# Kernel optimization log

Hardware: AMD Instinct MI355X
Metric: run time of the kernel (lower is better)

## Reference

```python
import jax, jax.numpy as jnp
import numpy as np

N, E, F_IN, H, F_OUT = 50000, 400000, 128, 256, 1
EPS = 1e-5


def setup_inputs() -> dict:
    key = jax.random.key(0)
    ks = jax.random.split(key, 10)
    s = lambda fan_in: 1.0 / np.sqrt(fan_in)
    return {
        "x": jax.random.normal(ks[0], (N, F_IN), dtype=jnp.float32),
        "edge_index": jax.random.randint(ks[1], (2, E), 0, N, dtype=jnp.int64),
        # gcn1: GCNConv(F_IN -> H) + BatchNorm1d(H) params
        "W1": jax.random.uniform(ks[2], (F_IN, H), jnp.float32, -s(F_IN), s(F_IN)),
        "b1": jnp.zeros((H,), jnp.float32),
        "gamma": jnp.ones((H,), jnp.float32),
        "beta": jnp.zeros((H,), jnp.float32),
        # gcn2: GCNConv(H -> H)
        "W2": jax.random.uniform(ks[3], (H, H), jnp.float32, -s(H), s(H)),
        "b2": jnp.zeros((H,), jnp.float32),
        # ClassifierMLP2(2H -> F_OUT): Linear(2H, H) -> ReLU -> Linear(H, F_OUT)
        "Wm1": jax.random.uniform(ks[4], (2 * H, H), jnp.float32, -s(2 * H), s(2 * H)),
        "bm1": jnp.zeros((H,), jnp.float32),
        "Wm2": jax.random.uniform(ks[5], (H, F_OUT), jnp.float32, -s(H), s(H)),
        "bm2": jnp.zeros((F_OUT,), jnp.float32),
    }


def _gcn_conv(x, W, b, src_full, dst_full, norm):
    # x' = D^{-1/2} (A + I) D^{-1/2} X W + b   (self loops already appended)
    xw = x @ W                                  # [N, H]
    msg = xw[src_full] * norm[:, None]          # [E+N, H] gather + scale
    agg = jax.ops.segment_sum(msg, dst_full, num_segments=N)  # scatter-add
    return agg + b


def reference(x, edge_index, W1, b1, gamma, beta, W2, b2, Wm1, bm1, Wm2, bm2):
    src, dst = edge_index[0], edge_index[1]
    loop = jnp.arange(N, dtype=edge_index.dtype)
    src_full = jnp.concatenate([src, loop])     # add_self_loops
    dst_full = jnp.concatenate([dst, loop])
    deg = jax.ops.segment_sum(jnp.ones_like(dst_full, dtype=x.dtype), dst_full,
                              num_segments=N)   # degree of A + I (>= 1)
    dinv = jax.lax.rsqrt(deg)
    norm = dinv[src_full] * dinv[dst_full]      # [E+N] symmetric norm

    # gcn1: conv -> batchnorm (batch stats) -> relu
    h = _gcn_conv(x, W1, b1, src_full, dst_full, norm)
    mu = jnp.mean(h, axis=0)
    var = jnp.mean(jnp.square(h - mu), axis=0)  # biased var, as in BN forward
    h = (h - mu) * jax.lax.rsqrt(var + EPS) * gamma + beta
    h = jax.nn.relu(h)

    # gcn2: conv -> relu
    h = jax.nn.relu(_gcn_conv(h, W2, b2, src_full, dst_full, norm))

    # mix_node_features 'cat': per-edge concat of endpoint features
    edges_x = jnp.concatenate([h[src], h[dst]], axis=-1)  # [E, 2H]

    # ClassifierMLP2 + sigmoid
    out = jax.nn.relu(edges_x @ Wm1 + bm1) @ Wm2 + bm2
    return jax.nn.sigmoid(out)                  # [E, 1]
```

## Files before the change

### kernel.cpp

```cpp
#include <hip/hip_runtime.h>
#include <math.h>

#define NN 50000
#define EE 400000
#define FIN 128
#define HH 256
#define BN_EPS 1e-5f
#define NSB 196

typedef __attribute__((ext_vector_type(8))) short short8v;
typedef __attribute__((ext_vector_type(4))) short short4v;
typedef __attribute__((ext_vector_type(2))) short short2v;
typedef __attribute__((ext_vector_type(4))) float f32x4;

__device__ inline short f2bf(float x) {
    union { float f; unsigned u; } c; c.f = x;
    unsigned r = c.u + 0x7FFF + ((c.u >> 16) & 1);
    return (short)(r >> 16);
}
__device__ inline float bf2f(short b) {
    union { unsigned u; float f; } c; c.u = ((unsigned)(unsigned short)b) << 16;
    return c.f;
}


__global__ void k_count(const int* __restrict__ dst, int* __restrict__ cnt) {
    int e = blockIdx.x * 256 + threadIdx.x;
    if (e < EE) atomicAdd(&cnt[dst[e]], 1);
}

__global__ __launch_bounds__(256) void k_scan1(const int* __restrict__ cnt,
                                               int* __restrict__ bsum) {
    __shared__ int ws4[4];
    int i = blockIdx.x * 256 + threadIdx.x;
    int s = (i < NN) ? cnt[i] : 0;
#pragma unroll
    for (int o = 32; o; o >>= 1) s += __shfl_down(s, o);
    if ((threadIdx.x & 63) == 0) ws4[threadIdx.x >> 6] = s;
    __syncthreads();
    if (threadIdx.x == 0) bsum[blockIdx.x] = ws4[0] + ws4[1] + ws4[2] + ws4[3];
}

__global__ __launch_bounds__(256) void k_scan2(const int* __restrict__ bsum,
                                               int* __restrict__ boff,
                                               int* __restrict__ row_start) {
    __shared__ int sh[256];
    int t = threadIdx.x;
    int v = (t < NSB) ? bsum[t] : 0;
    sh[t] = v;
    __syncthreads();
    for (int o = 1; o < 256; o <<= 1) {
        int u = (t >= o) ? sh[t - o] : 0;
        __syncthreads();
        sh[t] += u;
        __syncthreads();
    }
    if (t < NSB) boff[t] = sh[t] - v;
    if (t == 0) row_start[NN] = EE;
}

__global__ __launch_bounds__(256) void k_scan3(const int* __restrict__ cnt,
                                               const int* __restrict__ boff,
                                               int* __restrict__ row_start,
                                               int* __restrict__ cursor,
                                               float* __restrict__ dinv) {
    __shared__ int sh[256];
    int t = threadIdx.x;
    int i = blockIdx.x * 256 + t;
    int v = (i < NN) ? cnt[i] : 0;
    sh[t] = v;
    __syncthreads();
    for (int o = 1; o < 256; o <<= 1) {
        int u = (t >= o) ? sh[t - o] : 0;
        __syncthreads();
        sh[t] += u;
        __syncthreads();
    }
    if (i < NN) {
        int rs = boff[blockIdx.x] + sh[t] - v;
        row_start[i] = rs;
        cursor[i] = rs;
        dinv[i] = rsqrtf((float)(v + 1));
    }
}

__global__ void k_fill(const int* __restrict__ src, const int* __restrict__ dst,
                       int* __restrict__ cursor, int* __restrict__ csr_src) {
    int e = blockIdx.x * 256 + threadIdx.x;
    if (e < EE) {
        int pos = atomicAdd(&cursor[dst[e]], 1);
        csr_src[pos] = src[e];
    }
}


__global__ void k_wsplit(const float* __restrict__ src, short* __restrict__ hi,
                         short* __restrict__ lo, int K, int NC) {
    int i = blockIdx.x * 256 + threadIdx.x;
    if (i >= K * NC) return;
    int k = i / NC, n = i - k * NC;
    float v = src[i];
    short h = f2bf(v);
    short lw = f2bf(v - bf2f(h));
    size_t d = ((size_t)(k >> 3) * NC + n) * 8 + (k & 7);
    hi[d] = h;
    lo[d] = lw;
}

__global__ void k_wsplit_cat(const float* __restrict__ Wm1, short* __restrict__ hi,
                             short* __restrict__ lo) {
    int i = blockIdx.x * 256 + threadIdx.x;
    if (i >= 256 * 512) return;
    int k = i >> 9, c = i & 511;
    float v = (c < 256) ? Wm1[k * 256 + c] : Wm1[(256 + k) * 256 + (c - 256)];
    short h = f2bf(v);
    short lw = f2bf(v - bf2f(h));
    size_t d = ((size_t)(k >> 3) * 512 + c) * 8 + (k & 7);
    hi[d] = h;
    lo[d] = lw;
}


__global__ __launch_bounds__(256) void k_aggX(const float* __restrict__ x,
                                              const int* __restrict__ csr_src,
                                              const int* __restrict__ row_start,
                                              const float* __restrict__ dinv,
                                              short* __restrict__ Ghi,
                                              short* __restrict__ Glo) {
    int wave = threadIdx.x >> 6, lane = threadIdx.x & 63;
    int n = blockIdx.x * 4 + wave;
    if (n >= NN) return;
    const float2* base = reinterpret_cast<const float2*>(x);
    float g = dinv[n];
    float2 v = base[(size_t)n * 64 + lane];
    v.x *= g; v.y *= g;
    int s0 = row_start[n], s1 = row_start[n + 1];
    for (int j = s0; j < s1; ++j) {
        int sj = csr_src[j];
        float gj = dinv[sj];
        float2 u = base[(size_t)sj * 64 + lane];
        v.x += gj * u.x; v.y += gj * u.y;
    }
    v.x *= g; v.y *= g;
    short2v h, lw;
    short h0 = f2bf(v.x), h1 = f2bf(v.y);
    h[0] = h0; h[1] = h1;
    lw[0] = f2bf(v.x - bf2f(h0)); lw[1] = f2bf(v.y - bf2f(h1));
    *(short2v*)(Ghi + (size_t)n * FIN + lane * 2) = h;
    *(short2v*)(Glo + (size_t)n * FIN + lane * 2) = lw;
}

__global__ __launch_bounds__(256) void k_aggH(const float* __restrict__ T,
                                              const int* __restrict__ csr_src,
                                              const int* __restrict__ row_start,
                                              const float* __restrict__ dinv,
                                              short* __restrict__ Ghi,
                                              short* __restrict__ Glo) {
    int wave = threadIdx.x >> 6, lane = threadIdx.x & 63;
    int n = blockIdx.x * 4 + wave;
    if (n >= NN) return;
    const float4* base = reinterpret_cast<const float4*>(T);
    float4 v = base[(size_t)n * 64 + lane];
    int s0 = row_start[n], s1 = row_start[n + 1];
    for (int j = s0; j < s1; ++j) {
        float4 u = base[(size_t)csr_src[j] * 64 + lane];
        v.x += u.x; v.y += u.y; v.z += u.z; v.w += u.w;
    }
    float g = dinv[n];
    float o[4] = {v.x * g, v.y * g, v.z * g, v.w * g};
    short4v h, lw;
#pragma unroll
    for (int j = 0; j < 4; ++j) {
        short hh = f2bf(o[j]);
        h[j] = hh;
        lw[j] = f2bf(o[j] - bf2f(hh));
    }
    *(short4v*)(Ghi + (size_t)n * HH + lane * 4) = h;
    *(short4v*)(Glo + (size_t)n * HH + lane * 4) = lw;
}


template<int K, int NC, int EPI>
__global__ __launch_bounds__(256, 2) void gemm_stripe(
    const short* __restrict__ Ahi, const short* __restrict__ Alo,
    const short* __restrict__ Bthi, const short* __restrict__ Btlo,
    const float* __restrict__ bias,
    float* __restrict__ OutF, short* __restrict__ OutH, short* __restrict__ OutL,
    short* __restrict__ OutA, short* __restrict__ OutB2, int M)
{
    constexpr int NKT = K / 32;
    constexpr int NSLAB = K / 8;
    constexpr int NPASS = NC / 64;
    __shared__ short lds[2 * NSLAB * 512];
    const int tid = threadIdx.x;
    const int w = tid >> 6, l = tid & 63;
    const int wr = w >> 1, wc = w & 1;
    const int m0 = blockIdx.x * 64;
    const int lhi = l >> 4, llo = l & 15;

    for (int s = w; s < 2 * NSLAB; s += 4) {
        int kg = (s < NSLAB) ? s : (s - NSLAB);
        const short* srcp = (s < NSLAB) ? Ahi : Alo;
        int row = m0 + l;
        if (row > M - 1) row = M - 1;
        short8v v = *(const short8v*)(srcp + (size_t)row * K + kg * 8);
        *(short8v*)(&lds[s * 512 + l * 8]) = v;
    }
    __syncthreads();

    for (int pass = 0; pass < NPASS; ++pass) {
        const int n0 = pass * 64 + wc * 32;
        f32x4 acc[2][2] = {};
#pragma unroll
        for (int kt = 0; kt < NKT; ++kt) {
            short8v bh[2], bl[2];
#pragma unroll
            for (int nt = 0; nt < 2; ++nt) {
                size_t idx = ((size_t)(kt * 4 + lhi) * NC + (n0 + nt * 16 + llo)) * 8;
                bh[nt] = *(const short8v*)(Bthi + idx);
                bl[nt] = *(const short8v*)(Btlo + idx);
            }
            short8v ah[2], al[2];
#pragma unroll
            for (int mt = 0; mt < 2; ++mt) {
                int off = (kt * 4 + lhi) * 512 + (wr * 32 + mt * 16 + llo) * 8;
                ah[mt] = *(const short8v*)(&lds[off]);
                al[mt] = *(const short8v*)(&lds[off + NSLAB * 512]);
            }
#pragma unroll
            for (int mt = 0; mt < 2; ++mt)
#pragma unroll
                for (int nt = 0; nt < 2; ++nt) {
                    acc[mt][nt] = __builtin_amdgcn_mfma_f32_16x16x32_bf16(ah[mt], bh[nt], acc[mt][nt], 0, 0, 0);
                    acc[mt][nt] = __builtin_amdgcn_mfma_f32_16x16x32_bf16(ah[mt], bl[nt], acc[mt][nt], 0, 0, 0);
                    acc[mt][nt] = __builtin_amdgcn_mfma_f32_16x16x32_bf16(al[mt], bh[nt], acc[mt][nt], 0, 0, 0);
                }
        }
#pragma unroll
        for (int mt = 0; mt < 2; ++mt)
#pragma unroll
            for (int r = 0; r < 4; ++r) {
                int gm = m0 + wr * 32 + mt * 16 + lhi * 4 + r;
                if (gm >= M) continue;
#pragma unroll
                for (int nt = 0; nt < 2; ++nt) {
                    int col = n0 + nt * 16 + llo;
                    float v = acc[mt][nt][r];
                    if constexpr (EPI == 0) {
                        OutF[(size_t)gm * NC + col] = v + bias[col];
                    } else if constexpr (EPI == 1) {
                        float o = fmaxf(v + bias[col], 0.0f);
                        short h = f2bf(o);
                        OutH[(size_t)gm * NC + col] = h;
                        OutL[(size_t)gm * NC + col] = f2bf(o - bf2f(h));
                    } else {
                        short h = f2bf(v);
                        if (col < NC / 2)
                            OutA[(size_t)gm * (NC / 2) + col] = h;
                        else
                            OutB2[(size_t)gm * (NC / 2) + col - NC / 2] = h;
                    }
                }
            }
    }
}


__global__ __launch_bounds__(256) void k_bn_stats(const float* __restrict__ Hm,
                                                  float* __restrict__ ssum,
                                                  float* __restrict__ ssq) {
    int c = threadIdx.x;
    int r0 = blockIdx.x * 64;
    int r1 = min(r0 + 64, NN);
    float s = 0.f, q = 0.f;
    for (int r = r0; r < r1; ++r) {
        float v = Hm[(size_t)r * HH + c];
        s += v;
        q += v * v;
    }
    atomicAdd(&ssum[c], s);
    atomicAdd(&ssq[c], q);
}

__global__ void k_bn_final(const float* __restrict__ ssum, const float* __restrict__ ssq,
                           const float* __restrict__ gamma, const float* __restrict__ beta,
                           float* __restrict__ scale, float* __restrict__ shift) {
    int c = threadIdx.x;
    float mu = ssum[c] / (float)NN;
    float var = ssq[c] / (float)NN - mu * mu;
    float rstd = rsqrtf(var + BN_EPS);
    float sc = rstd * gamma[c];
    scale[c] = sc;
    shift[c] = beta[c] - mu * sc;
}

__global__ void k_bn_apply_T(const float* __restrict__ P1, const float* __restrict__ scale,
                             const float* __restrict__ shift, const float* __restrict__ dinv,
                             float* __restrict__ T) {
    int i4 = blockIdx.x * 256 + threadIdx.x;
    if (i4 >= NN * HH / 4) return;
    int c4 = i4 & 63;
    float g = dinv[i4 >> 6];
    float4 v = reinterpret_cast<const float4*>(P1)[i4];
    float4 sc = reinterpret_cast<const float4*>(scale)[c4];
    float4 sh = reinterpret_cast<const float4*>(shift)[c4];
    v.x = g * fmaxf(v.x * sc.x + sh.x, 0.f);
    v.y = g * fmaxf(v.y * sc.y + sh.y, 0.f);
    v.z = g * fmaxf(v.z * sc.z + sh.z, 0.f);
    v.w = g * fmaxf(v.w * sc.w + sh.w, 0.f);
    reinterpret_cast<float4*>(T)[i4] = v;
}


__global__ __launch_bounds__(256) void k_edge(const short* __restrict__ Aarr,
                                              const short* __restrict__ Barr,
                                              const int* __restrict__ src,
                                              const int* __restrict__ dst,
                                              const float* __restrict__ bm1,
                                              const float* __restrict__ Wm2,
                                              const float* __restrict__ bm2,
                                              float* __restrict__ out) {
    int wave = threadIdx.x >> 6;
    int lane = threadIdx.x & 63;
    int e = blockIdx.x * 4 + wave;
    if (e >= EE) return;
    int s = src[e], d = dst[e];
    short4v a = *(const short4v*)(Aarr + (size_t)s * 256 + lane * 4);
    short4v b = *(const short4v*)(Barr + (size_t)d * 256 + lane * 4);
    float4 bb = reinterpret_cast<const float4*>(bm1)[lane];
    float4 w = reinterpret_cast<const float4*>(Wm2)[lane];
    float t = fmaxf(bf2f(a[0]) + bf2f(b[0]) + bb.x, 0.f) * w.x
            + fmaxf(bf2f(a[1]) + bf2f(b[1]) + bb.y, 0.f) * w.y
            + fmaxf(bf2f(a[2]) + bf2f(b[2]) + bb.z, 0.f) * w.z
            + fmaxf(bf2f(a[3]) + bf2f(b[3]) + bb.w, 0.f) * w.w;
#pragma unroll
    for (int off = 32; off; off >>= 1) t += __shfl_xor(t, off);
    if (lane == 0) {
        float z = t + bm2[0];
        out[e] = 1.0f / (1.0f + expf(-z));
    }
}


extern "C" void kernel_launch(void* const* d_in, const int* in_sizes, int n_in,
                              void* d_out, int out_size, void* d_ws, size_t ws_size,
                              hipStream_t stream) {
    const float* x     = (const float*)d_in[0];
    const int*   ei    = (const int*)d_in[1];
    const float* W1    = (const float*)d_in[2];
    const float* b1    = (const float*)d_in[3];
    const float* gamma = (const float*)d_in[4];
    const float* beta  = (const float*)d_in[5];
    const float* W2    = (const float*)d_in[6];
    const float* b2    = (const float*)d_in[7];
    const float* Wm1   = (const float*)d_in[8];
    const float* bm1   = (const float*)d_in[9];
    const float* Wm2   = (const float*)d_in[10];
    const float* bm2   = (const float*)d_in[11];
    float* out = (float*)d_out;
    const int* src = ei;
    const int* dst = ei + EE;

    char* ws = (char*)d_ws;
    size_t off = 0;
    auto take = [&](size_t b) -> char* {
        char* p = ws + off;
        off += (b + 255) & ~(size_t)255;
        return p;
    };
    int*   deg_cnt   = (int*)take((size_t)NN * 4);
    float* dinv      = (float*)take((size_t)NN * 4);
    int*   row_start = (int*)take((size_t)(NN + 1) * 4);
    int*   cursor    = (int*)take((size_t)NN * 4);
    int*   csr_src   = (int*)take((size_t)EE * 4);
    int*   bsum      = (int*)take((size_t)NSB * 4);
    int*   boff      = (int*)take((size_t)NSB * 4);
    float* ssum      = (float*)take(1024);
    float* ssq       = (float*)take(1024);
    float* scale     = (float*)take(1024);
    float* shift     = (float*)take(1024);
    short* W1thi     = (short*)take((size_t)128 * 256 * 2);
    short* W1tlo     = (short*)take((size_t)128 * 256 * 2);
    short* W2thi     = (short*)take((size_t)256 * 256 * 2);
    short* W2tlo     = (short*)take((size_t)256 * 256 * 2);
    short* Wcthi     = (short*)take((size_t)256 * 512 * 2);
    short* Wctlo     = (short*)take((size_t)256 * 512 * 2);
    const size_t SLOT = (size_t)NN * HH * 4;
    char* slotA = take(SLOT);
    char* slotB = take(SLOT);
    char* slotC = take(SLOT);

    short* G1hi = (short*)slotB;
    short* G1lo = (short*)(slotB + 12800000);
    float* P1   = (float*)slotC;
    float* T    = (float*)slotA;
    short* G2hi = (short*)slotB;
    short* G2lo = (short*)(slotB + 25600000);
    short* H2hi = (short*)slotC;
    short* H2lo = (short*)(slotC + 25600000);
    short* Aarr = (short*)slotA;
    short* Barr = (short*)(slotA + 25600000);
    (void)ssq; (void)ws_size;

    hipMemsetAsync(deg_cnt, 0, (size_t)NN * 4, stream);
    hipMemsetAsync(ssum, 0, 2048, stream);

    k_count<<<(EE + 255) / 256, 256, 0, stream>>>(dst, deg_cnt);
    k_scan1<<<NSB, 256, 0, stream>>>(deg_cnt, bsum);
    k_scan2<<<1, 256, 0, stream>>>(bsum, boff, row_start);
    k_scan3<<<NSB, 256, 0, stream>>>(deg_cnt, boff, row_start, cursor, dinv);
    k_fill<<<(EE + 255) / 256, 256, 0, stream>>>(src, dst, cursor, csr_src);
    k_wsplit<<<(128 * 256 + 255) / 256, 256, 0, stream>>>(W1, W1thi, W1tlo, 128, 256);
    k_wsplit<<<(256 * 256 + 255) / 256, 256, 0, stream>>>(W2, W2thi, W2tlo, 256, 256);
    k_wsplit_cat<<<(256 * 512 + 255) / 256, 256, 0, stream>>>(Wm1, Wcthi, Wctlo);

    const int MB = (NN + 63) / 64;
    k_aggX<<<(NN + 3) / 4, 256, 0, stream>>>(x, csr_src, row_start, dinv, G1hi, G1lo);
    gemm_stripe<128, 256, 0><<<MB, 256, 0, stream>>>(G1hi, G1lo, W1thi, W1tlo, b1,
                                                     P1, nullptr, nullptr, nullptr, nullptr, NN);
    k_bn_stats<<<(NN + 63) / 64, 256, 0, stream>>>(P1, ssum, ssq);
    k_bn_final<<<1, 256, 0, stream>>>(ssum, ssq, gamma, beta, scale, shift);
    k_bn_apply_T<<<NN * HH / 4 / 256, 256, 0, stream>>>(P1, scale, shift, dinv, T);
    k_aggH<<<(NN + 3) / 4, 256, 0, stream>>>(T, csr_src, row_start, dinv, G2hi, G2lo);
    gemm_stripe<256, 256, 1><<<MB, 256, 0, stream>>>(G2hi, G2lo, W2thi, W2tlo, b2,
                                                     nullptr, H2hi, H2lo, nullptr, nullptr, NN);
    gemm_stripe<256, 512, 2><<<MB, 256, 0, stream>>>(H2hi, H2lo, Wcthi, Wctlo, nullptr,
                                                     nullptr, nullptr, nullptr, Aarr, Barr, NN);
    k_edge<<<(EE + 3) / 4, 256, 0, stream>>>(Aarr, Barr, src, dst, bm1, Wm2, bm2, out);
}
```

Measured before the change: 546.0 us.

## Store CSR edge ids, iterate edges per destination node, shrink GEMM row tile

The CSR now stores original edge ids instead of source ids, so the final edge classifier can walk edges grouped by destination node. The destination-side projection and bias are then loaded once per node instead of once per edge. The GEMM row tile drops from 64 to 32 rows, with each of four waves covering a 32-column stripe, and launch bounds are raised to target higher occupancy. The cost is an extra indirection (srcl[csr_eid[j]]) in both aggregation kernels and scattered per-edge output writes.

Result: slower. 677.6 us (+24.1%).

```diff
diff --git a/kernel.cpp b/kernel.cpp
--- a/kernel.cpp
+++ b/kernel.cpp
@@ -84,12 +84,12 @@
     }
 }
 
-__global__ void k_fill(const int* __restrict__ src, const int* __restrict__ dst,
-                       int* __restrict__ cursor, int* __restrict__ csr_src) {
+__global__ void k_fill(const int* __restrict__ dst,
+                       int* __restrict__ cursor, int* __restrict__ csr_eid) {
     int e = blockIdx.x * 256 + threadIdx.x;
     if (e < EE) {
         int pos = atomicAdd(&cursor[dst[e]], 1);
-        csr_src[pos] = src[e];
+        csr_eid[pos] = e;
     }
 }
 
@@ -122,7 +122,8 @@
 
 
 __global__ __launch_bounds__(256) void k_aggX(const float* __restrict__ x,
-                                              const int* __restrict__ csr_src,
+                                              const int* __restrict__ srcl,
+                                              const int* __restrict__ csr_eid,
                                               const int* __restrict__ row_start,
                                               const float* __restrict__ dinv,
                                               short* __restrict__ Ghi,
@@ -136,7 +137,7 @@
     v.x *= g; v.y *= g;
     int s0 = row_start[n], s1 = row_start[n + 1];
     for (int j = s0; j < s1; ++j) {
-        int sj = csr_src[j];
+        int sj = srcl[csr_eid[j]];
         float gj = dinv[sj];
         float2 u = base[(size_t)sj * 64 + lane];
         v.x += gj * u.x; v.y += gj * u.y;
@@ -151,7 +152,8 @@
 }
 
 __global__ __launch_bounds__(256) void k_aggH(const float* __restrict__ T,
-                                              const int* __restrict__ csr_src,
+                                              const int* __restrict__ srcl,
+                                              const int* __restrict__ csr_eid,
                                               const int* __restrict__ row_start,
                                               const float* __restrict__ dinv,
                                               short* __restrict__ Ghi,
@@ -163,7 +165,8 @@
     float4 v = base[(size_t)n * 64 + lane];
     int s0 = row_start[n], s1 = row_start[n + 1];
     for (int j = s0; j < s1; ++j) {
-        float4 u = base[(size_t)csr_src[j] * 64 + lane];
+        int sj = srcl[csr_eid[j]];
+        float4 u = base[(size_t)sj * 64 + lane];
         v.x += u.x; v.y += u.y; v.z += u.z; v.w += u.w;
     }
     float g = dinv[n];
@@ -181,7 +184,7 @@
 
 
 template<int K, int NC, int EPI>
-__global__ __launch_bounds__(256, 2) void gemm_stripe(
+__global__ __launch_bounds__(256, 4) void gemm_stripe(
     const short* __restrict__ Ahi, const short* __restrict__ Alo,
     const short* __restrict__ Bthi, const short* __restrict__ Btlo,
     const float* __restrict__ bias,
@@ -190,26 +193,27 @@
 {
     constexpr int NKT = K / 32;
     constexpr int NSLAB = K / 8;
-    constexpr int NPASS = NC / 64;
-    __shared__ short lds[2 * NSLAB * 512];
+    constexpr int NPASS = NC / 128;
+    __shared__ short lds[2 * NSLAB * 32 * 8];
     const int tid = threadIdx.x;
     const int w = tid >> 6, l = tid & 63;
-    const int wr = w >> 1, wc = w & 1;
-    const int m0 = blockIdx.x * 64;
+    const int m0 = blockIdx.x * 32;
     const int lhi = l >> 4, llo = l & 15;
 
-    for (int s = w; s < 2 * NSLAB; s += 4) {
-        int kg = (s < NSLAB) ? s : (s - NSLAB);
-        const short* srcp = (s < NSLAB) ? Ahi : Alo;
-        int row = m0 + l;
-        if (row > M - 1) row = M - 1;
-        short8v v = *(const short8v*)(srcp + (size_t)row * K + kg * 8);
-        *(short8v*)(&lds[s * 512 + l * 8]) = v;
+    for (int idx = tid; idx < 2 * NSLAB * 32; idx += 256) {
+        int buf = (idx >= NSLAB * 32) ? 1 : 0;
+        int rem = idx - buf * (NSLAB * 32);
+        int kg = rem >> 5, row = rem & 31;
+        const short* srcp = buf ? Alo : Ahi;
+        int r = m0 + row;
+        if (r > M - 1) r = M - 1;
+        short8v v = *(const short8v*)(srcp + (size_t)r * K + kg * 8);
+        *(short8v*)(&lds[idx * 8]) = v;
     }
     __syncthreads();
 
     for (int pass = 0; pass < NPASS; ++pass) {
-        const int n0 = pass * 64 + wc * 32;
+        const int n0 = pass * 128 + w * 32;
         f32x4 acc[2][2] = {};
 #pragma unroll
         for (int kt = 0; kt < NKT; ++kt) {
@@ -223,9 +227,9 @@
             short8v ah[2], al[2];
 #pragma unroll
             for (int mt = 0; mt < 2; ++mt) {
-                int off = (kt * 4 + lhi) * 512 + (wr * 32 + mt * 16 + llo) * 8;
+                int off = ((kt * 4 + lhi) * 32 + mt * 16 + llo) * 8;
                 ah[mt] = *(const short8v*)(&lds[off]);
-                al[mt] = *(const short8v*)(&lds[off + NSLAB * 512]);
+                al[mt] = *(const short8v*)(&lds[off + NSLAB * 32 * 8]);
             }
 #pragma unroll
             for (int mt = 0; mt < 2; ++mt)
@@ -240,7 +244,7 @@
         for (int mt = 0; mt < 2; ++mt)
 #pragma unroll
             for (int r = 0; r < 4; ++r) {
-                int gm = m0 + wr * 32 + mt * 16 + lhi * 4 + r;
+                int gm = m0 + mt * 16 + lhi * 4 + r;
                 if (gm >= M) continue;
 #pragma unroll
                 for (int nt = 0; nt < 2; ++nt) {
@@ -312,32 +316,37 @@
 }
 
 
-__global__ __launch_bounds__(256) void k_edge(const short* __restrict__ Aarr,
-                                              const short* __restrict__ Barr,
-                                              const int* __restrict__ src,
-                                              const int* __restrict__ dst,
-                                              const float* __restrict__ bm1,
-                                              const float* __restrict__ Wm2,
-                                              const float* __restrict__ bm2,
-                                              float* __restrict__ out) {
+__global__ __launch_bounds__(256) void k_edge_csr(const short* __restrict__ Aarr,
+                                                  const short* __restrict__ Barr,
+                                                  const int* __restrict__ srcl,
+                                                  const int* __restrict__ csr_eid,
+                                                  const int* __restrict__ row_start,
+                                                  const float* __restrict__ bm1,
+                                                  const float* __restrict__ Wm2,
+                                                  const float* __restrict__ bm2,
+                                                  float* __restrict__ out) {
     int wave = threadIdx.x >> 6;
     int lane = threadIdx.x & 63;
-    int e = blockIdx.x * 4 + wave;
-    if (e >= EE) return;
-    int s = src[e], d = dst[e];
-    short4v a = *(const short4v*)(Aarr + (size_t)s * 256 + lane * 4);
-    short4v b = *(const short4v*)(Barr + (size_t)d * 256 + lane * 4);
+    int n = blockIdx.x * 4 + wave;
+    if (n >= NN) return;
     float4 bb = reinterpret_cast<const float4*>(bm1)[lane];
     float4 w = reinterpret_cast<const float4*>(Wm2)[lane];
-    float t = fmaxf(bf2f(a[0]) + bf2f(b[0]) + bb.x, 0.f) * w.x
-            + fmaxf(bf2f(a[1]) + bf2f(b[1]) + bb.y, 0.f) * w.y
-            + fmaxf(bf2f(a[2]) + bf2f(b[2]) + bb.z, 0.f) * w.z
-            + fmaxf(bf2f(a[3]) + bf2f(b[3]) + bb.w, 0.f) * w.w;
-#pragma unroll
-    for (int off = 32; off; off >>= 1) t += __shfl_xor(t, off);
-    if (lane == 0) {
-        float z = t + bm2[0];
-        out[e] = 1.0f / (1.0f + expf(-z));
+    short4v bv = *(const short4v*)(Barr + (size_t)n * 256 + lane * 4);
+    float b0 = bf2f(bv[0]) + bb.x, b1 = bf2f(bv[1]) + bb.y,
+          b2 = bf2f(bv[2]) + bb.z, b3 = bf2f(bv[3]) + bb.w;
+    float zb = bm2[0];
+    int s0 = row_start[n], s1 = row_start[n + 1];
+    for (int j = s0; j < s1; ++j) {
+        int e = csr_eid[j];
+        int s = srcl[e];
+        short4v a = *(const short4v*)(Aarr + (size_t)s * 256 + lane * 4);
+        float t = fmaxf(bf2f(a[0]) + b0, 0.f) * w.x
+                + fmaxf(bf2f(a[1]) + b1, 0.f) * w.y
+                + fmaxf(bf2f(a[2]) + b2, 0.f) * w.z
+                + fmaxf(bf2f(a[3]) + b3, 0.f) * w.w;
+#pragma unroll
+        for (int off = 32; off; off >>= 1) t += __shfl_xor(t, off);
+        if (lane == 0) out[e] = 1.0f / (1.0f + expf(-(t + zb)));
     }
 }
 
@@ -372,7 +381,7 @@
     float* dinv      = (float*)take((size_t)NN * 4);
     int*   row_start = (int*)take((size_t)(NN + 1) * 4);
     int*   cursor    = (int*)take((size_t)NN * 4);
-    int*   csr_src   = (int*)take((size_t)EE * 4);
+    int*   csr_eid   = (int*)take((size_t)EE * 4);
     int*   bsum      = (int*)take((size_t)NSB * 4);
     int*   boff      = (int*)take((size_t)NSB * 4);
     float* ssum      = (float*)take(1024);
@@ -409,22 +418,23 @@
     k_scan1<<<NSB, 256, 0, stream>>>(deg_cnt, bsum);
     k_scan2<<<1, 256, 0, stream>>>(bsum, boff, row_start);
     k_scan3<<<NSB, 256, 0, stream>>>(deg_cnt, boff, row_start, cursor, dinv);
-    k_fill<<<(EE + 255) / 256, 256, 0, stream>>>(src, dst, cursor, csr_src);
+    k_fill<<<(EE + 255) / 256, 256, 0, stream>>>(dst, cursor, csr_eid);
     k_wsplit<<<(128 * 256 + 255) / 256, 256, 0, stream>>>(W1, W1thi, W1tlo, 128, 256);
     k_wsplit<<<(256 * 256 + 255) / 256, 256, 0, stream>>>(W2, W2thi, W2tlo, 256, 256);
     k_wsplit_cat<<<(256 * 512 + 255) / 256, 256, 0, stream>>>(Wm1, Wcthi, Wctlo);
 
-    const int MB = (NN + 63) / 64;
-    k_aggX<<<(NN + 3) / 4, 256, 0, stream>>>(x, csr_src, row_start, dinv, G1hi, G1lo);
-    gemm_stripe<128, 256, 0><<<MB, 256, 0, stream>>>(G1hi, G1lo, W1thi, W1tlo, b1,
-                                                     P1, nullptr, nullptr, nullptr, nullptr, NN);
+    const int MB32 = (NN + 31) / 32;
+    k_aggX<<<(NN + 3) / 4, 256, 0, stream>>>(x, src, csr_eid, row_start, dinv, G1hi, G1lo);
+    gemm_stripe<128, 256, 0><<<MB32, 256, 0, stream>>>(G1hi, G1lo, W1thi, W1tlo, b1,
+                                                       P1, nullptr, nullptr, nullptr, nullptr, NN);
     k_bn_stats<<<(NN + 63) / 64, 256, 0, stream>>>(P1, ssum, ssq);
     k_bn_final<<<1, 256, 0, stream>>>(ssum, ssq, gamma, beta, scale, shift);
     k_bn_apply_T<<<NN * HH / 4 / 256, 256, 0, stream>>>(P1, scale, shift, dinv, T);
-    k_aggH<<<(NN + 3) / 4, 256, 0, stream>>>(T, csr_src, row_start, dinv, G2hi, G2lo);
-    gemm_stripe<256, 256, 1><<<MB, 256, 0, stream>>>(G2hi, G2lo, W2thi, W2tlo, b2,
-                                                     nullptr, H2hi, H2lo, nullptr, nullptr, NN);
-    gemm_stripe<256, 512, 2><<<MB, 256, 0, stream>>>(H2hi, H2lo, Wcthi, Wctlo, nullptr,
-                                                     nullptr, nullptr, nullptr, Aarr, Barr, NN);
-    k_edge<<<(EE + 3) / 4, 256, 0, stream>>>(Aarr, Barr, src, dst, bm1, Wm2, bm2, out);
-}
+    k_aggH<<<(NN + 3) / 4, 256, 0, stream>>>(T, src, csr_eid, row_start, dinv, G2hi, G2lo);
+    gemm_stripe<256, 256, 1><<<MB32, 256, 0, stream>>>(G2hi, G2lo, W2thi, W2tlo, b2,
+                                                       nullptr, H2hi, H2lo, nullptr, nullptr, NN);
+    gemm_stripe<256, 512, 2><<<MB32, 256, 0, stream>>>(H2hi, H2lo, Wcthi, Wctlo, nullptr,
+                                                       nullptr, nullptr, nullptr, Aarr, Barr, NN);
+    k_edge_csr<<<(NN + 3) / 4, 256, 0, stream>>>(Aarr, Barr, src, csr_eid, row_start,
+                                                 bm1, Wm2, bm2, out);
+}
```
